# Optimization experiments

Hardware: AMD Instinct MI355X
Metric: run time of the kernel (lower is better)

## Reference

```python
import jax, jax.numpy as jnp
import numpy as np
import math

B, T, C, H = 4, 2048, 1024, 16
HD = C // H


def setup_inputs() -> dict:
    key = jax.random.key(0)
    ks = jax.random.split(key, 9)
    s = 1.0 / math.sqrt(C)
    return {
        "x": jax.random.normal(ks[0], (B, T, C), dtype=jnp.float32),
        "wq": jax.random.normal(ks[1], (C, C), dtype=jnp.float32) * s,
        "bq": jnp.zeros((C,), dtype=jnp.float32),
        "wk": jax.random.normal(ks[2], (C, C), dtype=jnp.float32) * s,
        "bk": jnp.zeros((C,), dtype=jnp.float32),
        "wv": jax.random.normal(ks[3], (C, C), dtype=jnp.float32) * s,
        "bv": jnp.zeros((C,), dtype=jnp.float32),
        "wp": jax.random.normal(ks[4], (C, C), dtype=jnp.float32) * s,
        "bp": jnp.zeros((C,), dtype=jnp.float32),
    }


def reference(x, wq, bq, wk, bk, wv, bv, wp, bp):
    b, t, c = x.shape
    # torch Linear: y = x @ W.T + b
    q = (x @ wq.T + bq).reshape(b, t, H, HD).transpose(0, 2, 1, 3)  # (B,H,T,hd)
    k = (x @ wk.T + bk).reshape(b, t, H, HD).transpose(0, 2, 1, 3)
    v = (x @ wv.T + bv).reshape(b, t, H, HD).transpose(0, 2, 1, 3)
    # NOTE: source scales by 1/sqrt(k.size(-1)) AFTER k.transpose(-2,-1),
    # i.e. 1/sqrt(T), not 1/sqrt(head_dim). Faithfully reproduced.
    scale = 1.0 / math.sqrt(t)
    scores = jnp.einsum("bhqd,bhkd->bhqk", q, k) * scale  # (B,H,T,T)
    causal = jnp.tril(jnp.ones((t, t), dtype=bool))
    scores = jnp.where(causal[None, None, :, :], scores, -jnp.inf)
    att = jax.nn.softmax(scores, axis=-1)
    out = jnp.einsum("bhqk,bhkd->bhqd", att, v)  # (B,H,T,hd)
    out = out.transpose(0, 2, 1, 3).reshape(b, t, c)
    return out @ wp.T + bp
```

## Files before the change

### kernel.cpp

```cpp
#include <hip/hip_runtime.h>
#include <stdint.h>
#include <math.h>

#define TB 2048
#define CD 1024

typedef short s16x8 __attribute__((ext_vector_type(8)));
typedef unsigned short u16x4 __attribute__((ext_vector_type(4)));
typedef float f32x4 __attribute__((ext_vector_type(4)));

#define QSCALE 0.02209708691207961f

__device__ __forceinline__ unsigned short f2bf(float f) {
    union { float f; uint32_t u; } v; v.f = f;
    return (unsigned short)((v.u + 0x7fffu + ((v.u >> 16) & 1u)) >> 16);
}

__device__ __forceinline__ void gl_lds16(const void* g, void* l) {
    typedef const __attribute__((address_space(1))) unsigned int gu32;
    typedef __attribute__((address_space(3))) unsigned int lu32;
    __builtin_amdgcn_global_load_lds((gu32*)g, (lu32*)l, 16, 0, 0);
}

__global__ void cast_k(const float* __restrict__ src, unsigned short* __restrict__ dst, int n4) {
    int i = blockIdx.x * blockDim.x + threadIdx.x;
    if (i < n4) {
        float4 v = reinterpret_cast<const float4*>(src)[i];
        u16x4 o = { f2bf(v.x), f2bf(v.y), f2bf(v.z), f2bf(v.w) };
        reinterpret_cast<u16x4*>(dst)[i] = o;
    }
}

template<int MODE>
__launch_bounds__(256)
__global__ void gemm_bt(const unsigned short* __restrict__ A,
                        const unsigned short* __restrict__ Bw,
                        unsigned short* __restrict__ qo,
                        unsigned short* __restrict__ ko,
                        unsigned short* __restrict__ vto,
                        const float* __restrict__ b0,
                        const float* __restrict__ b1,
                        const float* __restrict__ b2,
                        float* __restrict__ fout,
                        const float* __restrict__ bp)
{
    __shared__ unsigned short As[128 * 32];
    __shared__ unsigned short Bs[128 * 32];
    const int tid = threadIdx.x;
    const int mbase = blockIdx.y * 128;
    const int nbase = blockIdx.x * 128;
    const int lane = tid & 63;
    const int w = tid >> 6;
    const int g = lane >> 4;
    const int lr = lane & 15;
    const int wm = (w >> 1) * 64;
    const int wn = (w & 1) * 64;
    const int srow = lane >> 2;
    const int scol = (lane & 3) * 8;

    f32x4 acc[4][4];
#pragma unroll
    for (int i = 0; i < 4; ++i)
#pragma unroll
        for (int j = 0; j < 4; ++j) acc[i][j] = (f32x4)0.0f;

    const size_t arow0 = (size_t)(mbase + w * 16 + srow);
    const size_t arow1 = (size_t)(mbase + 64 + w * 16 + srow);
    const size_t brow0 = (size_t)(nbase + w * 16 + srow);
    const size_t brow1 = (size_t)(nbase + 64 + w * 16 + srow);
    unsigned short* asd0 = As + (w * 16) * 32;
    unsigned short* asd1 = As + (64 + w * 16) * 32;
    unsigned short* bsd0 = Bs + (w * 16) * 32;
    unsigned short* bsd1 = Bs + (64 + w * 16) * 32;

    for (int k0 = 0; k0 < 1024; k0 += 32) {
        __syncthreads();
        gl_lds16(A  + arow0 * 1024 + k0 + scol, asd0);
        gl_lds16(A  + arow1 * 1024 + k0 + scol, asd1);
        gl_lds16(Bw + brow0 * 1024 + k0 + scol, bsd0);
        gl_lds16(Bw + brow1 * 1024 + k0 + scol, bsd1);
        __syncthreads();
        s16x8 af[4], bfv[4];
#pragma unroll
        for (int mi = 0; mi < 4; ++mi)
            af[mi] = *reinterpret_cast<const s16x8*>(&As[(wm + mi * 16 + lr) * 32 + g * 8]);
#pragma unroll
        for (int ni = 0; ni < 4; ++ni)
            bfv[ni] = *reinterpret_cast<const s16x8*>(&Bs[(wn + ni * 16 + lr) * 32 + g * 8]);
#pragma unroll
        for (int mi = 0; mi < 4; ++mi)
#pragma unroll
            for (int ni = 0; ni < 4; ++ni)
                acc[mi][ni] = __builtin_amdgcn_mfma_f32_16x16x32_bf16(af[mi], bfv[ni], acc[mi][ni], 0, 0, 0);
    }

#pragma unroll
    for (int mi = 0; mi < 4; ++mi) {
        const int mg = mbase + wm + mi * 16 + g * 4;
#pragma unroll
        for (int ni = 0; ni < 4; ++ni) {
            const int ng = nbase + wn + ni * 16 + lr;
            if constexpr (MODE == 0) {
                const int which = ng >> 10;
                const int nin = ng & 1023;
                const float bias = (which == 0) ? b0[nin] : (which == 1) ? b1[nin] : b2[nin];
                const int h = nin >> 6, d = nin & 63;
                const int b = mg >> 11, t = mg & 2047;
                if (which == 2) {
                    u16x4 pv = { f2bf(acc[mi][ni][0] + bias), f2bf(acc[mi][ni][1] + bias),
                                 f2bf(acc[mi][ni][2] + bias), f2bf(acc[mi][ni][3] + bias) };
                    *reinterpret_cast<u16x4*>(vto + ((size_t)((b * 16 + h) * 64 + d)) * 2048 + t) = pv;
                } else if (which == 0) {
#pragma unroll
                    for (int r = 0; r < 4; ++r)
                        qo[((size_t)(b * 16 + h) * 2048 + (t + r)) * 64 + d] =
                            f2bf((acc[mi][ni][r] + bias) * QSCALE);
                } else {
#pragma unroll
                    for (int r = 0; r < 4; ++r)
                        ko[((size_t)(b * 16 + h) * 2048 + (t + r)) * 64 + d] = f2bf(acc[mi][ni][r] + bias);
                }
            } else {
                const float bias = bp[ng];
#pragma unroll
                for (int r = 0; r < 4; ++r)
                    fout[(size_t)(mg + r) * 1024 + ng] = acc[mi][ni][r] + bias;
            }
        }
    }
}

__launch_bounds__(256, 2)
__global__ void attn_k(const unsigned short* __restrict__ qg,
                       const unsigned short* __restrict__ kg,
                       const unsigned short* __restrict__ vtg,
                       unsigned short* __restrict__ og)
{
    __shared__ unsigned short Kt[2][64 * 64];
    __shared__ unsigned short Vs[2][64 * 64];
    __shared__ unsigned short P_lds[4][32 * 64];

    const int pr = blockIdx.x;
    const int bh = blockIdx.y;
    const int b = bh >> 4, h = bh & 15;
    const int tid = threadIdx.x;
    const int w = tid >> 6;
    const int lane = tid & 63;
    const int g = lane >> 4;
    const int lr = lane & 15;

    const unsigned short* Qp = qg + (size_t)bh * TB * 64;
    const unsigned short* Kp = kg + (size_t)bh * TB * 64;
    const unsigned short* Vt = vtg + (size_t)bh * 64 * TB;
    unsigned short* Pw = P_lds[w];

    const int srow = lane >> 3;
    const int schk = lane & 7;
    const int gchk = schk ^ srow;
    const int seg0 = w * 2, seg1 = w * 2 + 1;
    const int swz = (lr & 7);

#pragma unroll 1
    for (int half = 0; half < 2; ++half) {
        const int sup = half == 0 ? pr : 15 - pr;
        const int qw = sup * 128 + w * 32;
        const int ntw = (qw >> 6) + 1;
        const int NT = sup * 2 + 2;

        s16x8 bq0[2], bq1[2];
#pragma unroll
        for (int qf = 0; qf < 2; ++qf) {
            const unsigned short* qp = Qp + (size_t)(qw + qf * 16 + lr) * 64 + g * 8;
            bq0[qf] = *reinterpret_cast<const s16x8*>(qp);
            bq1[qf] = *reinterpret_cast<const s16x8*>(qp + 32);
        }

        f32x4 oacc[4][2];
#pragma unroll
        for (int dt = 0; dt < 4; ++dt)
#pragma unroll
            for (int qf = 0; qf < 2; ++qf) oacc[dt][qf] = (f32x4)0.0f;
        float mi_[2] = { -INFINITY, -INFINITY };
        float li_[2] = { 0.0f, 0.0f };

        asm volatile("s_waitcnt lgkmcnt(0)" ::: "memory");
        __builtin_amdgcn_s_barrier();
        {
            gl_lds16(Kp + (size_t)(seg0 * 8 + srow) * 64 + gchk * 8, &Kt[0][seg0 * 512]);
            gl_lds16(Kp + (size_t)(seg1 * 8 + srow) * 64 + gchk * 8, &Kt[0][seg1 * 512]);
            gl_lds16(Vt + (size_t)(seg0 * 8 + srow) * TB + gchk * 8, &Vs[0][seg0 * 512]);
            gl_lds16(Vt + (size_t)(seg1 * 8 + srow) * TB + gchk * 8, &Vs[0][seg1 * 512]);
        }
        asm volatile("s_waitcnt vmcnt(0)" ::: "memory");
        __builtin_amdgcn_s_barrier();
        asm volatile("" ::: "memory");
        __builtin_amdgcn_sched_barrier(0);

        int cur = 0;
#pragma unroll 1
        for (int t = 0; t < NT; ++t) {
            const int other = cur ^ 1;
            if (t > 0) {
                asm volatile("s_waitcnt lgkmcnt(0)" ::: "memory");
                __builtin_amdgcn_s_barrier();
            }
            if (t + 1 < NT) {
                const int k0n = (t + 1) * 64;
                gl_lds16(Kp + (size_t)(k0n + seg0 * 8 + srow) * 64 + gchk * 8, &Kt[other][seg0 * 512]);
                gl_lds16(Kp + (size_t)(k0n + seg1 * 8 + srow) * 64 + gchk * 8, &Kt[other][seg1 * 512]);
                gl_lds16(Vt + (size_t)(seg0 * 8 + srow) * TB + k0n + gchk * 8, &Vs[other][seg0 * 512]);
                gl_lds16(Vt + (size_t)(seg1 * 8 + srow) * TB + k0n + gchk * 8, &Vs[other][seg1 * 512]);
                asm volatile("s_waitcnt vmcnt(4)" ::: "memory");
            } else {
                asm volatile("s_waitcnt vmcnt(0)" ::: "memory");
            }
            __builtin_amdgcn_s_barrier();
            asm volatile("" ::: "memory");
            __builtin_amdgcn_sched_barrier(0);

            if (t < ntw) {
                const unsigned short* Kc = Kt[cur];
                const unsigned short* Vc = Vs[cur];
                f32x4 st[4][2];
#pragma unroll
                for (int sub = 0; sub < 4; ++sub) {
                    const unsigned short* krow = Kc + (sub * 16 + lr) * 64;
                    s16x8 ak0 = *reinterpret_cast<const s16x8*>(krow + ((g ^ swz) * 8));
                    s16x8 ak1 = *reinterpret_cast<const s16x8*>(krow + (((g + 4) ^ swz) * 8));
#pragma unroll
                    for (int qf = 0; qf < 2; ++qf) {
                        f32x4 z = (f32x4)0.0f;
                        z = __builtin_amdgcn_mfma_f32_16x16x32_bf16(ak0, bq0[qf], z, 0, 0, 0);
                        st[sub][qf] = __builtin_amdgcn_mfma_f32_16x16x32_bf16(ak1, bq1[qf], z, 0, 0, 0);
                    }
                }
                if (t == ntw - 1) {
                    const int k0 = t * 64;
#pragma unroll
                    for (int sub = 0; sub < 4; ++sub)
#pragma unroll
                        for (int qf = 0; qf < 2; ++qf)
#pragma unroll
                            for (int r = 0; r < 4; ++r) {
                                const int key = k0 + sub * 16 + g * 4 + r;
                                const int q = qw + qf * 16 + lr;
                                if (key > q) st[sub][qf][r] = -INFINITY;
                            }
                }
                float alpha[2];
#pragma unroll
                for (int qf = 0; qf < 2; ++qf) {
                    float mloc = st[0][qf][0];
#pragma unroll
                    for (int sub = 0; sub < 4; ++sub)
#pragma unroll
                        for (int r = 0; r < 4; ++r) mloc = fmaxf(mloc, st[sub][qf][r]);
                    mloc = fmaxf(mloc, __shfl_xor(mloc, 16));
                    mloc = fmaxf(mloc, __shfl_xor(mloc, 32));
                    const float mn = fmaxf(mi_[qf], mloc);
                    alpha[qf] = __expf(mi_[qf] - mn);
                    mi_[qf] = mn;
                    float ps = 0.0f;
#pragma unroll
                    for (int sub = 0; sub < 4; ++sub)
#pragma unroll
                        for (int r = 0; r < 4; ++r) {
                            const float p = __expf(st[sub][qf][r] - mn);
                            st[sub][qf][r] = p;
                            ps += p;
                        }
                    ps += __shfl_xor(ps, 16);
                    ps += __shfl_xor(ps, 32);
                    li_[qf] = li_[qf] * alpha[qf] + ps;
                }
#pragma unroll
                for (int dt = 0; dt < 4; ++dt)
#pragma unroll
                    for (int qf = 0; qf < 2; ++qf) oacc[dt][qf] *= alpha[qf];
#pragma unroll
                for (int sub = 0; sub < 4; ++sub)
#pragma unroll
                    for (int qf = 0; qf < 2; ++qf) {
                        u16x4 pk = { f2bf(st[sub][qf][0]), f2bf(st[sub][qf][1]),
                                     f2bf(st[sub][qf][2]), f2bf(st[sub][qf][3]) };
                        const int row = qf * 16 + lr;
                        const int bo = sub * 32 + g * 8;
                        const int phys = ((bo >> 4) ^ (row & 7)) * 16 + (bo & 15);
                        *reinterpret_cast<u16x4*>(reinterpret_cast<char*>(Pw + row * 64) + phys) = pk;
                    }
                s16x8 vf[8];
#pragma unroll
                for (int dt = 0; dt < 4; ++dt)
#pragma unroll
                    for (int ks = 0; ks < 2; ++ks)
                        vf[dt * 2 + ks] = *reinterpret_cast<const s16x8*>(
                            Vc + (dt * 16 + lr) * 64 + (((ks * 4 + g) ^ swz) * 8));
#pragma unroll
                for (int qf = 0; qf < 2; ++qf)
#pragma unroll
                    for (int ks = 0; ks < 2; ++ks) {
                        const int row = qf * 16 + lr;
                        const int gran = (ks * 4 + g) ^ (row & 7);
                        s16x8 pb = *reinterpret_cast<const s16x8*>(
                            reinterpret_cast<const char*>(Pw + row * 64) + gran * 16);
#pragma unroll
                        for (int dt = 0; dt < 4; ++dt)
                            oacc[dt][qf] = __builtin_amdgcn_mfma_f32_16x16x32_bf16(vf[dt * 2 + ks], pb, oacc[dt][qf], 0, 0, 0);
                    }
            }
            cur = other;
        }

#pragma unroll
        for (int qf = 0; qf < 2; ++qf) {
            const float inv_l = 1.0f / li_[qf];
            unsigned short* orow = og + ((size_t)(b * TB + qw + qf * 16 + lr)) * CD + h * 64;
#pragma unroll
            for (int dt = 0; dt < 4; ++dt) {
                u16x4 ov = { f2bf(oacc[dt][qf][0] * inv_l), f2bf(oacc[dt][qf][1] * inv_l),
                             f2bf(oacc[dt][qf][2] * inv_l), f2bf(oacc[dt][qf][3] * inv_l) };
                *reinterpret_cast<u16x4*>(orow + dt * 16 + g * 4) = ov;
            }
        }
    }
}

extern "C" void kernel_launch(void* const* d_in, const int* in_sizes, int n_in,
                              void* d_out, int out_size, void* d_ws, size_t ws_size,
                              hipStream_t stream)
{
    const float* x  = (const float*)d_in[0];
    const float* wq = (const float*)d_in[1];
    const float* bq = (const float*)d_in[2];
    const float* wk = (const float*)d_in[3];
    const float* bk = (const float*)d_in[4];
    const float* wv = (const float*)d_in[5];
    const float* bv = (const float*)d_in[6];
    const float* wp = (const float*)d_in[7];
    const float* bp = (const float*)d_in[8];
    float* out = (float*)d_out;

    unsigned short* xb   = (unsigned short*)d_ws;
    unsigned short* wcat = xb + 8388608;
    unsigned short* wpb  = wcat + 3145728;
    unsigned short* qb_  = wpb + 1048576;
    unsigned short* kb_  = qb_ + 8388608;
    unsigned short* vtb  = kb_ + 8388608;
    unsigned short* ob   = xb;

    cast_k<<<8192, 256, 0, stream>>>(x, xb, 2097152);
    cast_k<<<1024, 256, 0, stream>>>(wq, wcat, 262144);
    cast_k<<<1024, 256, 0, stream>>>(wk, wcat + 1048576, 262144);
    cast_k<<<1024, 256, 0, stream>>>(wv, wcat + 2097152, 262144);
    cast_k<<<1024, 256, 0, stream>>>(wp, wpb, 262144);

    gemm_bt<0><<<dim3(24, 64), 256, 0, stream>>>(xb, wcat, qb_, kb_, vtb,
                                                 bq, bk, bv, nullptr, nullptr);
    attn_k<<<dim3(8, 64), 256, 0, stream>>>(qb_, kb_, vtb, ob);
    gemm_bt<1><<<dim3(8, 64), 256, 0, stream>>>(ob, wpb, nullptr, nullptr, nullptr,
                                                nullptr, nullptr, nullptr, out, bp);
}
```

Before: 300.2 us.

## Use 8 waves of 16 query rows in attention with lazy softmax rescaling

The attention kernel now runs 512 threads per block, and each wave handles 16 query rows instead of 32. This halves per-wave register state and spreads each K/V tile load across 8 waves. The online softmax only rescales the accumulator when the running max grows by more than a threshold, which skips exp and multiply work on most tiles. V fragments are loaded inside the MFMA loop instead of being preloaded, and the bf16 conversion now uses the library intrinsic. In exchange, each K/V tile in LDS is reused by fewer query rows per wave and there are more waves to synchronize at barriers.

Measured after the change: 274.8 us. 1.09x faster.

```diff
diff --git a/kernel.cpp b/kernel.cpp
--- a/kernel.cpp
+++ b/kernel.cpp
@@ -1,4 +1,5 @@
 #include <hip/hip_runtime.h>
+#include <hip/hip_bf16.h>
 #include <stdint.h>
 #include <math.h>
 
@@ -12,8 +13,8 @@
 #define QSCALE 0.02209708691207961f
 
 __device__ __forceinline__ unsigned short f2bf(float f) {
-    union { float f; uint32_t u; } v; v.f = f;
-    return (unsigned short)((v.u + 0x7fffu + ((v.u >> 16) & 1u)) >> 16);
+    __hip_bfloat16 h = __float2bfloat16(f);
+    return reinterpret_cast<unsigned short&>(h);
 }
 
 __device__ __forceinline__ void gl_lds16(const void* g, void* l) {
@@ -130,7 +131,7 @@
     }
 }
 
-__launch_bounds__(256, 2)
+__launch_bounds__(512, 4)
 __global__ void attn_k(const unsigned short* __restrict__ qg,
                        const unsigned short* __restrict__ kg,
                        const unsigned short* __restrict__ vtg,
@@ -138,7 +139,7 @@
 {
     __shared__ unsigned short Kt[2][64 * 64];
     __shared__ unsigned short Vs[2][64 * 64];
-    __shared__ unsigned short P_lds[4][32 * 64];
+    __shared__ unsigned short P_lds[8][16 * 64];
 
     const int pr = blockIdx.x;
     const int bh = blockIdx.y;
@@ -157,40 +158,28 @@
     const int srow = lane >> 3;
     const int schk = lane & 7;
     const int gchk = schk ^ srow;
-    const int seg0 = w * 2, seg1 = w * 2 + 1;
-    const int swz = (lr & 7);
+    const int swz = lr & 7;
 
 #pragma unroll 1
     for (int half = 0; half < 2; ++half) {
         const int sup = half == 0 ? pr : 15 - pr;
-        const int qw = sup * 128 + w * 32;
+        const int qw = sup * 128 + w * 16;
         const int ntw = (qw >> 6) + 1;
         const int NT = sup * 2 + 2;
 
-        s16x8 bq0[2], bq1[2];
-#pragma unroll
-        for (int qf = 0; qf < 2; ++qf) {
-            const unsigned short* qp = Qp + (size_t)(qw + qf * 16 + lr) * 64 + g * 8;
-            bq0[qf] = *reinterpret_cast<const s16x8*>(qp);
-            bq1[qf] = *reinterpret_cast<const s16x8*>(qp + 32);
-        }
-
-        f32x4 oacc[4][2];
-#pragma unroll
-        for (int dt = 0; dt < 4; ++dt)
-#pragma unroll
-            for (int qf = 0; qf < 2; ++qf) oacc[dt][qf] = (f32x4)0.0f;
-        float mi_[2] = { -INFINITY, -INFINITY };
-        float li_[2] = { 0.0f, 0.0f };
+        const unsigned short* qp = Qp + (size_t)(qw + lr) * 64 + g * 8;
+        s16x8 bq0 = *reinterpret_cast<const s16x8*>(qp);
+        s16x8 bq1 = *reinterpret_cast<const s16x8*>(qp + 32);
+
+        f32x4 oacc[4];
+#pragma unroll
+        for (int dt = 0; dt < 4; ++dt) oacc[dt] = (f32x4)0.0f;
+        float mi_ = -INFINITY, li_ = 0.0f;
 
         asm volatile("s_waitcnt lgkmcnt(0)" ::: "memory");
         __builtin_amdgcn_s_barrier();
-        {
-            gl_lds16(Kp + (size_t)(seg0 * 8 + srow) * 64 + gchk * 8, &Kt[0][seg0 * 512]);
-            gl_lds16(Kp + (size_t)(seg1 * 8 + srow) * 64 + gchk * 8, &Kt[0][seg1 * 512]);
-            gl_lds16(Vt + (size_t)(seg0 * 8 + srow) * TB + gchk * 8, &Vs[0][seg0 * 512]);
-            gl_lds16(Vt + (size_t)(seg1 * 8 + srow) * TB + gchk * 8, &Vs[0][seg1 * 512]);
-        }
+        gl_lds16(Kp + (size_t)(w * 8 + srow) * 64 + gchk * 8, &Kt[0][w * 512]);
+        gl_lds16(Vt + (size_t)(w * 8 + srow) * TB + gchk * 8, &Vs[0][w * 512]);
         asm volatile("s_waitcnt vmcnt(0)" ::: "memory");
         __builtin_amdgcn_s_barrier();
         asm volatile("" ::: "memory");
@@ -206,11 +195,9 @@
             }
             if (t + 1 < NT) {
                 const int k0n = (t + 1) * 64;
-                gl_lds16(Kp + (size_t)(k0n + seg0 * 8 + srow) * 64 + gchk * 8, &Kt[other][seg0 * 512]);
-                gl_lds16(Kp + (size_t)(k0n + seg1 * 8 + srow) * 64 + gchk * 8, &Kt[other][seg1 * 512]);
-                gl_lds16(Vt + (size_t)(seg0 * 8 + srow) * TB + k0n + gchk * 8, &Vs[other][seg0 * 512]);
-                gl_lds16(Vt + (size_t)(seg1 * 8 + srow) * TB + k0n + gchk * 8, &Vs[other][seg1 * 512]);
-                asm volatile("s_waitcnt vmcnt(4)" ::: "memory");
+                gl_lds16(Kp + (size_t)(k0n + w * 8 + srow) * 64 + gchk * 8, &Kt[other][w * 512]);
+                gl_lds16(Vt + (size_t)(w * 8 + srow) * TB + k0n + gchk * 8, &Vs[other][w * 512]);
+                asm volatile("s_waitcnt vmcnt(2)" ::: "memory");
             } else {
                 asm volatile("s_waitcnt vmcnt(0)" ::: "memory");
             }
@@ -221,106 +208,84 @@
             if (t < ntw) {
                 const unsigned short* Kc = Kt[cur];
                 const unsigned short* Vc = Vs[cur];
-                f32x4 st[4][2];
+                f32x4 st[4];
 #pragma unroll
                 for (int sub = 0; sub < 4; ++sub) {
                     const unsigned short* krow = Kc + (sub * 16 + lr) * 64;
                     s16x8 ak0 = *reinterpret_cast<const s16x8*>(krow + ((g ^ swz) * 8));
                     s16x8 ak1 = *reinterpret_cast<const s16x8*>(krow + (((g + 4) ^ swz) * 8));
-#pragma unroll
-                    for (int qf = 0; qf < 2; ++qf) {
-                        f32x4 z = (f32x4)0.0f;
-                        z = __builtin_amdgcn_mfma_f32_16x16x32_bf16(ak0, bq0[qf], z, 0, 0, 0);
-                        st[sub][qf] = __builtin_amdgcn_mfma_f32_16x16x32_bf16(ak1, bq1[qf], z, 0, 0, 0);
-                    }
+                    f32x4 z = (f32x4)0.0f;
+                    z = __builtin_amdgcn_mfma_f32_16x16x32_bf16(ak0, bq0, z, 0, 0, 0);
+                    st[sub] = __builtin_amdgcn_mfma_f32_16x16x32_bf16(ak1, bq1, z, 0, 0, 0);
                 }
                 if (t == ntw - 1) {
                     const int k0 = t * 64;
 #pragma unroll
                     for (int sub = 0; sub < 4; ++sub)
 #pragma unroll
-                        for (int qf = 0; qf < 2; ++qf)
-#pragma unroll
-                            for (int r = 0; r < 4; ++r) {
-                                const int key = k0 + sub * 16 + g * 4 + r;
-                                const int q = qw + qf * 16 + lr;
-                                if (key > q) st[sub][qf][r] = -INFINITY;
-                            }
-                }
-                float alpha[2];
-#pragma unroll
-                for (int qf = 0; qf < 2; ++qf) {
-                    float mloc = st[0][qf][0];
-#pragma unroll
-                    for (int sub = 0; sub < 4; ++sub)
-#pragma unroll
-                        for (int r = 0; r < 4; ++r) mloc = fmaxf(mloc, st[sub][qf][r]);
-                    mloc = fmaxf(mloc, __shfl_xor(mloc, 16));
-                    mloc = fmaxf(mloc, __shfl_xor(mloc, 32));
-                    const float mn = fmaxf(mi_[qf], mloc);
-                    alpha[qf] = __expf(mi_[qf] - mn);
-                    mi_[qf] = mn;
-                    float ps = 0.0f;
-#pragma unroll
-                    for (int sub = 0; sub < 4; ++sub)
-#pragma unroll
                         for (int r = 0; r < 4; ++r) {
-                            const float p = __expf(st[sub][qf][r] - mn);
-                            st[sub][qf][r] = p;
-                            ps += p;
+                            const int key = k0 + sub * 16 + g * 4 + r;
+                            if (key > qw + lr) st[sub][r] = -INFINITY;
                         }
-                    ps += __shfl_xor(ps, 16);
-                    ps += __shfl_xor(ps, 32);
-                    li_[qf] = li_[qf] * alpha[qf] + ps;
-                }
-#pragma unroll
-                for (int dt = 0; dt < 4; ++dt)
-#pragma unroll
-                    for (int qf = 0; qf < 2; ++qf) oacc[dt][qf] *= alpha[qf];
+                }
+                float mloc = st[0][0];
 #pragma unroll
                 for (int sub = 0; sub < 4; ++sub)
 #pragma unroll
-                    for (int qf = 0; qf < 2; ++qf) {
-                        u16x4 pk = { f2bf(st[sub][qf][0]), f2bf(st[sub][qf][1]),
-                                     f2bf(st[sub][qf][2]), f2bf(st[sub][qf][3]) };
-                        const int row = qf * 16 + lr;
-                        const int bo = sub * 32 + g * 8;
-                        const int phys = ((bo >> 4) ^ (row & 7)) * 16 + (bo & 15);
-                        *reinterpret_cast<u16x4*>(reinterpret_cast<char*>(Pw + row * 64) + phys) = pk;
+                    for (int r = 0; r < 4; ++r) mloc = fmaxf(mloc, st[sub][r]);
+                mloc = fmaxf(mloc, __shfl_xor(mloc, 16));
+                mloc = fmaxf(mloc, __shfl_xor(mloc, 32));
+                if (__any(mloc - mi_ > 8.0f)) {
+                    const float mn = fmaxf(mi_, mloc);
+                    const float alpha = __expf(mi_ - mn);
+                    li_ *= alpha;
+#pragma unroll
+                    for (int dt = 0; dt < 4; ++dt) oacc[dt] *= alpha;
+                    mi_ = mn;
+                }
+                float ps = 0.0f;
+#pragma unroll
+                for (int sub = 0; sub < 4; ++sub)
+#pragma unroll
+                    for (int r = 0; r < 4; ++r) {
+                        const float p = __expf(st[sub][r] - mi_);
+                        st[sub][r] = p;
+                        ps += p;
                     }
-                s16x8 vf[8];
-#pragma unroll
-                for (int dt = 0; dt < 4; ++dt)
-#pragma unroll
-                    for (int ks = 0; ks < 2; ++ks)
-                        vf[dt * 2 + ks] = *reinterpret_cast<const s16x8*>(
+                ps += __shfl_xor(ps, 16);
+                ps += __shfl_xor(ps, 32);
+                li_ += ps;
+#pragma unroll
+                for (int sub = 0; sub < 4; ++sub) {
+                    u16x4 pk = { f2bf(st[sub][0]), f2bf(st[sub][1]),
+                                 f2bf(st[sub][2]), f2bf(st[sub][3]) };
+                    const int bo = sub * 32 + g * 8;
+                    const int phys = ((bo >> 4) ^ swz) * 16 + (bo & 15);
+                    *reinterpret_cast<u16x4*>(reinterpret_cast<char*>(Pw + lr * 64) + phys) = pk;
+                }
+#pragma unroll
+                for (int ks = 0; ks < 2; ++ks) {
+                    const int gran = (ks * 4 + g) ^ swz;
+                    s16x8 pb = *reinterpret_cast<const s16x8*>(
+                        reinterpret_cast<const char*>(Pw + lr * 64) + gran * 16);
+#pragma unroll
+                    for (int dt = 0; dt < 4; ++dt) {
+                        s16x8 vfr = *reinterpret_cast<const s16x8*>(
                             Vc + (dt * 16 + lr) * 64 + (((ks * 4 + g) ^ swz) * 8));
-#pragma unroll
-                for (int qf = 0; qf < 2; ++qf)
-#pragma unroll
-                    for (int ks = 0; ks < 2; ++ks) {
-                        const int row = qf * 16 + lr;
-                        const int gran = (ks * 4 + g) ^ (row & 7);
-                        s16x8 pb = *reinterpret_cast<const s16x8*>(
-                            reinterpret_cast<const char*>(Pw + row * 64) + gran * 16);
-#pragma unroll
-                        for (int dt = 0; dt < 4; ++dt)
-                            oacc[dt][qf] = __builtin_amdgcn_mfma_f32_16x16x32_bf16(vf[dt * 2 + ks], pb, oacc[dt][qf], 0, 0, 0);
+                        oacc[dt] = __builtin_amdgcn_mfma_f32_16x16x32_bf16(vfr, pb, oacc[dt], 0, 0, 0);
                     }
+                }
             }
             cur = other;
         }
 
-#pragma unroll
-        for (int qf = 0; qf < 2; ++qf) {
-            const float inv_l = 1.0f / li_[qf];
-            unsigned short* orow = og + ((size_t)(b * TB + qw + qf * 16 + lr)) * CD + h * 64;
-#pragma unroll
-            for (int dt = 0; dt < 4; ++dt) {
-                u16x4 ov = { f2bf(oacc[dt][qf][0] * inv_l), f2bf(oacc[dt][qf][1] * inv_l),
-                             f2bf(oacc[dt][qf][2] * inv_l), f2bf(oacc[dt][qf][3] * inv_l) };
-                *reinterpret_cast<u16x4*>(orow + dt * 16 + g * 4) = ov;
-            }
+        const float inv_l = 1.0f / li_;
+        unsigned short* orow = og + ((size_t)(b * TB + qw + lr)) * CD + h * 64;
+#pragma unroll
+        for (int dt = 0; dt < 4; ++dt) {
+            u16x4 ov = { f2bf(oacc[dt][0] * inv_l), f2bf(oacc[dt][1] * inv_l),
+                         f2bf(oacc[dt][2] * inv_l), f2bf(oacc[dt][3] * inv_l) };
+            *reinterpret_cast<u16x4*>(orow + dt * 16 + g * 4) = ov;
         }
     }
 }
@@ -356,7 +321,7 @@
 
     gemm_bt<0><<<dim3(24, 64), 256, 0, stream>>>(xb, wcat, qb_, kb_, vtb,
                                                  bq, bk, bv, nullptr, nullptr);
-    attn_k<<<dim3(8, 64), 256, 0, stream>>>(qb_, kb_, vtb, ob);
+    attn_k<<<dim3(8, 64), 512, 0, stream>>>(qb_, kb_, vtb, ob);
     gemm_bt<1><<<dim3(8, 64), 256, 0, stream>>>(ob, wpb, nullptr, nullptr, nullptr,
                                                 nullptr, nullptr, nullptr, out, bp);
 }
```
